# Performance work log

Measured on AMD Instinct MI355X. Metric: run time of the kernel, lower is better.

Reference implementation:

```python
import jax, jax.numpy as jnp
import numpy as np

N = 1024  # step_num
M = 1024  # state_num
C = 64    # in_channels


def _mlp3(x, w1, b1, w2, b2, w3, b3):
    # LinearStack(3, C, C, out): Linear+ReLU, Linear+ReLU, Linear
    h = jax.nn.relu(x @ w1 + b1)
    h = jax.nn.relu(h @ w2 + b2)
    return h @ w3 + b3


def setup_inputs() -> dict:
    key = jax.random.key(0)
    ks = jax.random.split(key, 10)
    s = 1.0 / np.sqrt(C)
    return {
        'step_x': jax.random.normal(ks[0], (N, C), jnp.float32),
        'state_x': jax.random.normal(ks[1], (M, C), jnp.float32),
        'pre_w1': jax.random.normal(ks[2], (C, C), jnp.float32) * s,
        'pre_b1': jnp.zeros((C,), jnp.float32),
        'pre_w2': jax.random.normal(ks[3], (C, C), jnp.float32) * s,
        'pre_b2': jnp.zeros((C,), jnp.float32),
        'pre_w3': jax.random.normal(ks[4], (C, C), jnp.float32) * s,
        'pre_b3': jnp.zeros((C,), jnp.float32),
        'post_w1': jax.random.normal(ks[5], (C, C), jnp.float32) * s,
        'post_b1': jnp.zeros((C,), jnp.float32),
        'post_w2': jax.random.normal(ks[6], (C, C), jnp.float32) * s,
        'post_b2': jnp.zeros((C,), jnp.float32),
        'post_w3': jax.random.normal(ks[7], (C, 2), jnp.float32) * s,
        'post_b3': jnp.zeros((2,), jnp.float32),
    }


def reference(step_x, state_x,
              pre_w1, pre_b1, pre_w2, pre_b2, pre_w3, pre_b3,
              post_w1, post_b1, post_w2, post_b2, post_w3, post_b3):
    # pre-compare MLP on both node sets
    sx = _mlp3(step_x, pre_w1, pre_b1, pre_w2, pre_b2, pre_w3, pre_b3)   # [N,C]
    tx = _mlp3(state_x, pre_w1, pre_b1, pre_w2, pre_b2, pre_w3, pre_b3)  # [M,C]
    n, c = sx.shape
    m = tx.shape[0]

    # step-step pairwise compare ('add') + post-compare -> [N,N,2]
    pair_ss = (sx[:, None, :] + sx[None, :, :]).reshape(n * n, c)
    logits_ss = _mlp3(pair_ss, post_w1, post_b1, post_w2, post_b2,
                      post_w3, post_b3).reshape(n, n, 2)

    # step-state pairwise compare + post-compare -> [N,M,2]
    pair_st = (sx[:, None, :] + tx[None, :, :]).reshape(n * m, c)
    logits_st = _mlp3(pair_st, post_w1, post_b1, post_w2, post_b2,
                      post_w3, post_b3).reshape(n, m, 2)

    # mutual-argmax bipartite matching on sigmoid(match logits)
    match = jax.nn.sigmoid(logits_st[..., 0])                 # [N,M]
    col_arg = jnp.argmax(match, axis=0)                       # [M]
    mask_c = (jnp.arange(n)[:, None] == col_arg[None, :]).astype(match.dtype)
    s1 = match * mask_c
    row_arg = jnp.argmax(s1, axis=1)                          # [N]
    mask_r = (jnp.arange(m)[None, :] == row_arg[:, None]).astype(s1.dtype)
    matched_scores = s1 * mask_r                              # [N,M]

    return logits_ss, logits_st, matched_scores
```

## Files before the change

### kernel.cpp

```cpp
#include <hip/hip_runtime.h>
#include <math.h>

namespace {

constexpr int N_ = 1024;
constexpr int M_ = 1024;
constexpr int C_ = 64;

typedef _Float16 f16x8 __attribute__((ext_vector_type(8)));
typedef __fp16 fp16x2 __attribute__((ext_vector_type(2)));
typedef float f32x4 __attribute__((ext_vector_type(4)));
static_assert(sizeof(f16x8) == 16, "f16x8 must be 4 VGPRs");

__device__ __forceinline__ float sig(float x) { return 1.0f / (1.0f + expf(-x)); }

__device__ __forceinline__ unsigned flipbits(float f) {
    unsigned u = __float_as_uint(f);
    return u ^ (0x80000000u | (unsigned)((int)u >> 31));
}
__device__ __forceinline__ float unflipbits(unsigned k) {
    unsigned u = (k & 0x80000000u) ? (k ^ 0x80000000u) : ~k;
    return __uint_as_float(u);
}
__device__ __forceinline__ unsigned long long packlogit(float v, unsigned idx) {
    return ((unsigned long long)flipbits(v) << 32) | (unsigned)(0xFFFFFFFFu - idx);
}
__device__ __forceinline__ unsigned long long packpos(float v, unsigned idx) {
    return ((unsigned long long)__float_as_uint(v) << 32) | (unsigned)(0xFFFFFFFFu - idx);
}
__device__ __forceinline__ unsigned long long shflx64(unsigned long long v, int m) {
    unsigned lo = __shfl_xor((unsigned)v, m);
    unsigned hi = __shfl_xor((unsigned)(v >> 32), m);
    return ((unsigned long long)hi << 32) | lo;
}

__global__ __launch_bounds__(256) void pre_prep_kernel(
    const float* __restrict__ step_x, const float* __restrict__ state_x,
    const float* __restrict__ w1, const float* __restrict__ b1,
    const float* __restrict__ w2, const float* __restrict__ b2,
    const float* __restrict__ w3, const float* __restrict__ b3,
    const float* __restrict__ pw1, const float* __restrict__ pw2,
    float* __restrict__ U, _Float16* __restrict__ w2T,
    unsigned long long* __restrict__ rowbest)
{
    const int t = threadIdx.x;
    if (blockIdx.x == 128) {
        for (int e = t; e < C_ * C_; e += 256) {
            int k = e >> 6, c = e & 63;
            w2T[c * 64 + k] = (_Float16)pw2[e];
        }
        for (int e = t; e < 1024; e += 256) rowbest[e] = 0ull;
        return;
    }

    __shared__ float XA[16][C_ + 1];
    __shared__ float XB[16][C_ + 1];
    __shared__ float W[C_ * C_];
    __shared__ float Bv[C_];

    const int c = t & 63;
    const int rg = t >> 6;
    const int rbase = blockIdx.x * 16;

    const float* src_g = (rbase < N_) ? (step_x + (size_t)rbase * C_)
                                      : (state_x + (size_t)(rbase - N_) * C_);
    {
        int row = t >> 4, k4 = (t & 15) << 2;
        float4 v = *reinterpret_cast<const float4*>(src_g + row * C_ + k4);
        XA[row][k4 + 0] = v.x; XA[row][k4 + 1] = v.y;
        XA[row][k4 + 2] = v.z; XA[row][k4 + 3] = v.w;
    }

    const float* Ws[4] = {w1, w2, w3, pw1};
    const float* Bs[4] = {b1, b2, b3, nullptr};

    float (*sA)[C_ + 1] = XA;
    float (*sB)[C_ + 1] = XB;

    for (int layer = 0; layer < 4; ++layer) {
        __syncthreads();
        for (int e = t; e < C_ * C_ / 4; e += 256)
            reinterpret_cast<float4*>(W)[e] =
                reinterpret_cast<const float4*>(Ws[layer])[e];
        if (t < C_) Bv[t] = (layer == 3) ? 0.0f : Bs[layer][t];
        __syncthreads();
        const bool relu = (layer < 2);
        #pragma unroll
        for (int q = 0; q < 4; ++q) {
            const int row = rg * 4 + q;
            float acc = Bv[c];
            #pragma unroll 8
            for (int k = 0; k < C_; ++k)
                acc = fmaf(sA[row][k], W[k * C_ + c], acc);
            sB[row][c] = relu ? fmaxf(acc, 0.0f) : acc;
        }
        float (*tmp)[C_ + 1] = sA; sA = sB; sB = tmp;
    }
    #pragma unroll
    for (int q = 0; q < 4; ++q) {
        const int row = rg * 4 + q;
        U[(size_t)(rbase + row) * C_ + c] = sA[row][c];
    }
}

__global__ __launch_bounds__(256) void pair_kernel(
    const float* __restrict__ U,
    const _Float16* __restrict__ w2T,
    const float* __restrict__ pb1, const float* __restrict__ pb2,
    const float* __restrict__ pw3, const float* __restrict__ pb3,
    float* __restrict__ out, unsigned long long* __restrict__ PT2)
{
    __shared__ float SU[32][68];
    __shared__ float SVB[32][68];
    __shared__ float OUTT[32][33][2];
    __shared__ unsigned long long RED[8][32][2];

    const int t = threadIdx.x;
    const int lane = t & 63;
    const int wave = t >> 6;
    const int wi = wave >> 1, wj = wave & 1;
    const int zz = blockIdx.z;
    const int ibase = blockIdx.y * 32;
    const int jbase = blockIdx.x * 32;

    {
        int r = t >> 3, k0 = (t & 7) * 8;
        const float* up = U + (size_t)(ibase + r) * C_ + k0;
        *reinterpret_cast<float4*>(&SU[r][k0])     = *reinterpret_cast<const float4*>(up);
        *reinterpret_cast<float4*>(&SU[r][k0 + 4]) = *reinterpret_cast<const float4*>(up + 4);
        const float* vp = U + (size_t)((zz ? N_ : 0) + jbase + r) * C_ + k0;
        float4 b0 = *reinterpret_cast<const float4*>(vp);
        float4 b1v = *reinterpret_cast<const float4*>(vp + 4);
        float4 c0 = *reinterpret_cast<const float4*>(pb1 + k0);
        float4 c1 = *reinterpret_cast<const float4*>(pb1 + k0 + 4);
        b0.x += c0.x; b0.y += c0.y; b0.z += c0.z; b0.w += c0.w;
        b1v.x += c1.x; b1v.y += c1.y; b1v.z += c1.z; b1v.w += c1.w;
        *reinterpret_cast<float4*>(&SVB[r][k0])     = b0;
        *reinterpret_cast<float4*>(&SVB[r][k0 + 4]) = b1v;
    }

    const int ch_l = lane & 15;
    const int kg = lane >> 4;

    f16x8 whi[4][2];
    #pragma unroll
    for (int mt = 0; mt < 4; ++mt)
        #pragma unroll
        for (int ks = 0; ks < 2; ++ks)
            whi[mt][ks] = *reinterpret_cast<const f16x8*>(
                w2T + (mt * 16 + ch_l) * 64 + ks * 32 + kg * 8);

    float b2v[16], w30[16], w31[16];
    #pragma unroll
    for (int mt = 0; mt < 4; ++mt)
        #pragma unroll
        for (int r = 0; r < 4; ++r) {
            int ch = mt * 16 + kg * 4 + r;
            b2v[mt * 4 + r] = pb2[ch];
            w30[mt * 4 + r] = pw3[ch * 2];
            w31[mt * 4 + r] = pw3[ch * 2 + 1];
        }
    const float ob0 = pb3[0], ob1 = pb3[1];

    __syncthreads();

    float su[2][8];
    #pragma unroll
    for (int ks = 0; ks < 2; ++ks) {
        int k0 = ks * 32 + kg * 8;
        float4 a = *reinterpret_cast<const float4*>(&SU[wi * 16 + ch_l][k0]);
        float4 b = *reinterpret_cast<const float4*>(&SU[wi * 16 + ch_l][k0 + 4]);
        su[ks][0] = a.x; su[ks][1] = a.y; su[ks][2] = a.z; su[ks][3] = a.w;
        su[ks][4] = b.x; su[ks][5] = b.y; su[ks][6] = b.z; su[ks][7] = b.w;
    }

    for (int jj = 0; jj < 16; ++jj) {
        const int jr = wj * 16 + jj;
        f16x8 bhi[2];
        #pragma unroll
        for (int ks = 0; ks < 2; ++ks) {
            int k0 = ks * 32 + kg * 8;
            float4 a = *reinterpret_cast<const float4*>(&SVB[jr][k0]);
            float4 b = *reinterpret_cast<const float4*>(&SVB[jr][k0 + 4]);
            float sv[8] = {a.x, a.y, a.z, a.w, b.x, b.y, b.z, b.w};
            union { f16x8 v; fp16x2 h2[4]; } bu;
            #pragma unroll
            for (int m = 0; m < 4; ++m) {
                float x0 = fmaxf(su[ks][2 * m]     + sv[2 * m],     0.0f);
                float x1 = fmaxf(su[ks][2 * m + 1] + sv[2 * m + 1], 0.0f);
                bu.h2[m] = __builtin_amdgcn_cvt_pkrtz(x0, x1);
            }
            bhi[ks] = bu.v;
        }
        f32x4 ah[4];
        #pragma unroll
        for (int mt = 0; mt < 4; ++mt)
            ah[mt] = f32x4{b2v[4 * mt], b2v[4 * mt + 1], b2v[4 * mt + 2], b2v[4 * mt + 3]};
        #pragma unroll
        for (int ks = 0; ks < 2; ++ks)
            #pragma unroll
            for (int mt = 0; mt < 4; ++mt)
                ah[mt] = __builtin_amdgcn_mfma_f32_16x16x32_f16(whi[mt][ks], bhi[ks], ah[mt], 0, 0, 0);
        float p0 = 0.0f, p1 = 0.0f;
        #pragma unroll
        for (int mt = 0; mt < 4; ++mt)
            #pragma unroll
            for (int r = 0; r < 4; ++r) {
                float g = fmaxf(ah[mt][r], 0.0f);
                p0 = fmaf(g, w30[4 * mt + r], p0);
                p1 = fmaf(g, w31[4 * mt + r], p1);
            }
        p0 += __shfl_xor(p0, 16); p0 += __shfl_xor(p0, 32);
        p1 += __shfl_xor(p1, 16); p1 += __shfl_xor(p1, 32);
        if (lane < 16) {
            OUTT[wi * 16 + lane][wj * 16 + jj][0] = p0 + ob0;
            OUTT[wi * 16 + lane][wj * 16 + jj][1] = p1 + ob1;
        }
    }
    __syncthreads();
    {
        float* obase = out + (size_t)zz * (2ull * N_ * M_);
        int r = t >> 3;
        int q0 = (t & 7) * 4;
        int i = ibase + r;
        #pragma unroll
        for (int q = 0; q < 4; ++q) {
            int j = jbase + q0 + q;
            float2 v = *reinterpret_cast<float2*>(&OUTT[r][q0 + q][0]);
            *reinterpret_cast<float2*>(obase + ((size_t)i * M_ + j) * 2) = v;
        }
    }
    if (zz) {
        const int tc = t & 31, tg = t >> 5;
        unsigned long long k1 = 0, k2 = 0;
        #pragma unroll
        for (int q = 0; q < 4; ++q) {
            int r = tg * 4 + q;
            unsigned long long k = packlogit(OUTT[r][tc][0], (unsigned)(ibase + r));
            if (k > k1) { k2 = k1; k1 = k; } else if (k > k2) k2 = k;
        }
        RED[tg][tc][0] = k1; RED[tg][tc][1] = k2;
        for (int h = 4; h > 0; h >>= 1) {
            __syncthreads();
            if (tg < h) {
                unsigned long long a = RED[tg + h][tc][0], b = RED[tg + h][tc][1];
                if (a > k1) { k2 = k1; k1 = a; } else if (a > k2) k2 = a;
                if (b > k1) { k2 = k1; k1 = b; } else if (b > k2) k2 = b;
                RED[tg][tc][0] = k1; RED[tg][tc][1] = k2;
            }
        }
        if (tg == 0) {
            size_t o = ((size_t)blockIdx.y * M_ + (jbase + tc)) * 2;
            PT2[o] = k1; PT2[o + 1] = k2;
        }
    }
}

__global__ __launch_bounds__(64) void colfinal_kernel(
    const unsigned long long* __restrict__ PT2,
    const float* __restrict__ U, const float* __restrict__ pb1,
    const float* __restrict__ pw2, const float* __restrict__ pb2,
    const float* __restrict__ pw3, const float* __restrict__ pb3,
    unsigned long long* __restrict__ rowbest)
{
    __shared__ float h1s[64];
    const int j = blockIdx.x;
    const int lane = threadIdx.x;

    unsigned long long k1 = PT2[((size_t)(lane >> 1) * M_ + j) * 2 + (lane & 1)];
    unsigned long long k2 = 0;
    #pragma unroll
    for (int m = 1; m < 64; m <<= 1) {
        unsigned long long a = shflx64(k1, m), b = shflx64(k2, m);
        if (a > k1) { k2 = k1; k1 = a; } else if (a > k2) k2 = a;
        if (b > k1) { k2 = k1; k1 = b; } else if (b > k2) k2 = b;
    }
    int ids[2];
    ids[0] = (int)(0xFFFFFFFFu - (unsigned)(k1 & 0xFFFFFFFFull));
    ids[1] = (int)(0xFFFFFFFFu - (unsigned)(k2 & 0xFFFFFFFFull));
    float v1 = unflipbits((unsigned)(k1 >> 32));
    float v2 = unflipbits((unsigned)(k2 >> 32));
    const int nc = (v1 - v2 < 8e-3f) ? 2 : 1;

    float logits[2] = {0.0f, 0.0f};
    for (int cnd = 0; cnd < nc; ++cnd) {
        int i = ids[cnd];
        h1s[lane] = fmaxf(U[(size_t)i * C_ + lane] + U[(size_t)(N_ + j) * C_ + lane] + pb1[lane], 0.0f);
        __syncthreads();
        float acc = pb2[lane];
        #pragma unroll 8
        for (int k = 0; k < 64; ++k)
            acc = fmaf(h1s[k], pw2[k * 64 + lane], acc);
        float p = fmaxf(acc, 0.0f) * pw3[lane * 2];
        #pragma unroll
        for (int m = 1; m < 64; m <<= 1) p += __shfl_xor(p, m);
        logits[cnd] = p + pb3[0];
        __syncthreads();
    }
    int wi; float wp;
    if (nc == 1) { wi = ids[0]; wp = logits[0]; }
    else if (logits[0] > logits[1]) { wi = ids[0]; wp = logits[0]; }
    else if (logits[1] > logits[0]) { wi = ids[1]; wp = logits[1]; }
    else { wi = min(ids[0], ids[1]); wp = logits[0]; }
    if (lane == 0)
        atomicMax(&rowbest[wi], packpos(sig(wp), (unsigned)j));
}

__global__ __launch_bounds__(256) void zscatter_kernel(
    const unsigned long long* __restrict__ rowbest, float* __restrict__ matched)
{
    int i = blockIdx.x;
    int t = threadIdx.x;
    *reinterpret_cast<float4*>(matched + (size_t)i * M_ + t * 4) =
        float4{0.0f, 0.0f, 0.0f, 0.0f};
    __syncthreads();
    if (t == 0) {
        unsigned long long key = rowbest[i];
        if (key) {
            unsigned j = 0xFFFFFFFFu - (unsigned)(key & 0xFFFFFFFFull);
            matched[(size_t)i * M_ + j] = __uint_as_float((unsigned)(key >> 32));
        }
    }
}

}

extern "C" void kernel_launch(void* const* d_in, const int* in_sizes, int n_in,
                              void* d_out, int out_size, void* d_ws, size_t ws_size,
                              hipStream_t stream)
{
    const float* step_x  = (const float*)d_in[0];
    const float* state_x = (const float*)d_in[1];
    const float* pre_w1  = (const float*)d_in[2];
    const float* pre_b1  = (const float*)d_in[3];
    const float* pre_w2  = (const float*)d_in[4];
    const float* pre_b2  = (const float*)d_in[5];
    const float* pre_w3  = (const float*)d_in[6];
    const float* pre_b3  = (const float*)d_in[7];
    const float* post_w1 = (const float*)d_in[8];
    const float* post_b1 = (const float*)d_in[9];
    const float* post_w2 = (const float*)d_in[10];
    const float* post_b2 = (const float*)d_in[11];
    const float* post_w3 = (const float*)d_in[12];
    const float* post_b3 = (const float*)d_in[13];

    float* out     = (float*)d_out;
    float* matched = out + 4ull * N_ * M_;

    float* U = (float*)d_ws;
    unsigned long long* rowbest = (unsigned long long*)((char*)d_ws + 2048ull * 64 * 4);

    char* ms = (char*)matched;
    unsigned long long* PT2 = (unsigned long long*)ms;
    _Float16*  w2T     = (_Float16*)(ms + 512 * 1024);

    hipLaunchKernelGGL(pre_prep_kernel, dim3(129), dim3(256), 0, stream,
        step_x, state_x, pre_w1, pre_b1, pre_w2, pre_b2, pre_w3, pre_b3,
        post_w1, post_w2, U, w2T, rowbest);
    hipLaunchKernelGGL(pair_kernel, dim3(32, 32, 2), dim3(256), 0, stream,
        U, w2T, post_b1, post_b2, post_w3, post_b3, out, PT2);
    hipLaunchKernelGGL(colfinal_kernel, dim3(1024), dim3(64), 0, stream,
        PT2, U, post_b1, post_w2, post_b2, post_w3, post_b3, rowbest);
    hipLaunchKernelGGL(zscatter_kernel, dim3(1024), dim3(256), 0, stream,
        rowbest, matched);
}
```

Baseline: 147.2 us.

## Fuse all four stages into one persistent kernel with grid barriers

Merges the pre-MLP, pairwise MFMA, column-final and scatter kernels into a single 512-block persistent kernel separated by atomic grid-wide barriers, with a memset to clear barrier counters and rowbest. Each block now handles both the step-step and step-state tiles for a shared U row tile, reusing the loaded SU data, and colfinal packs four columns per block. The aim is to remove launch gaps and tail effects between the small kernels. In exchange it relies on all 512 blocks being co-resident for the spin barriers, and it lowers parallelism in the pre-MLP and pair stages. The colfinal step also now always evaluates two candidates instead of branching on the gap.

Measured after the change: 427.1 us. 2.9x slower.

```diff
diff --git a/kernel.cpp b/kernel.cpp
--- a/kernel.cpp
+++ b/kernel.cpp
@@ -6,11 +6,11 @@
 constexpr int N_ = 1024;
 constexpr int M_ = 1024;
 constexpr int C_ = 64;
+constexpr unsigned NBLK = 512;
 
 typedef _Float16 f16x8 __attribute__((ext_vector_type(8)));
 typedef __fp16 fp16x2 __attribute__((ext_vector_type(2)));
 typedef float f32x4 __attribute__((ext_vector_type(4)));
-static_assert(sizeof(f16x8) == 16, "f16x8 must be 4 VGPRs");
 
 __device__ __forceinline__ float sig(float x) { return 1.0f / (1.0f + expf(-x)); }
 
@@ -34,291 +34,298 @@
     return ((unsigned long long)hi << 32) | lo;
 }
 
-__global__ __launch_bounds__(256) void pre_prep_kernel(
+__device__ __forceinline__ void gridbar(unsigned* bar, unsigned target) {
+    __syncthreads();
+    if (threadIdx.x == 0) {
+        __threadfence();
+        __hip_atomic_fetch_add(bar, 1u, __ATOMIC_RELEASE, __HIP_MEMORY_SCOPE_AGENT);
+        while (__hip_atomic_load(bar, __ATOMIC_ACQUIRE, __HIP_MEMORY_SCOPE_AGENT) < target)
+            __builtin_amdgcn_s_sleep(4);
+        __threadfence();
+    }
+    __syncthreads();
+}
+
+struct SmemA { float XA[4][C_ + 1]; float XB[4][C_ + 1]; float W[C_ * C_]; float Bv[C_]; };
+struct SmemB {
+    float SU[32][68];
+    float SVB[2][32][68];
+    float OUTT[32][33][2];
+    unsigned long long RED[8][32][2];
+};
+struct SmemC { float h1s[4][C_]; };
+union Smem { SmemA a; SmemB b; SmemC c; };
+
+__global__ __launch_bounds__(256, 4) void fused_kernel(
     const float* __restrict__ step_x, const float* __restrict__ state_x,
     const float* __restrict__ w1, const float* __restrict__ b1,
     const float* __restrict__ w2, const float* __restrict__ b2,
     const float* __restrict__ w3, const float* __restrict__ b3,
-    const float* __restrict__ pw1, const float* __restrict__ pw2,
+    const float* __restrict__ pw1, const float* __restrict__ pb1,
+    const float* __restrict__ pw2, const float* __restrict__ pb2,
+    const float* __restrict__ pw3, const float* __restrict__ pb3,
     float* __restrict__ U, _Float16* __restrict__ w2T,
-    unsigned long long* __restrict__ rowbest)
+    unsigned long long* __restrict__ rowbest,
+    float* __restrict__ out, unsigned long long* __restrict__ PT2,
+    unsigned* __restrict__ bar)
 {
+    __shared__ Smem sm;
     const int t = threadIdx.x;
-    if (blockIdx.x == 128) {
-        for (int e = t; e < C_ * C_; e += 256) {
-            int k = e >> 6, c = e & 63;
-            w2T[c * 64 + k] = (_Float16)pw2[e];
-        }
-        for (int e = t; e < 1024; e += 256) rowbest[e] = 0ull;
-        return;
-    }
-
-    __shared__ float XA[16][C_ + 1];
-    __shared__ float XB[16][C_ + 1];
-    __shared__ float W[C_ * C_];
-    __shared__ float Bv[C_];
-
-    const int c = t & 63;
-    const int rg = t >> 6;
-    const int rbase = blockIdx.x * 16;
-
-    const float* src_g = (rbase < N_) ? (step_x + (size_t)rbase * C_)
-                                      : (state_x + (size_t)(rbase - N_) * C_);
+    const int bid = blockIdx.x;
+
     {
-        int row = t >> 4, k4 = (t & 15) << 2;
-        float4 v = *reinterpret_cast<const float4*>(src_g + row * C_ + k4);
-        XA[row][k4 + 0] = v.x; XA[row][k4 + 1] = v.y;
-        XA[row][k4 + 2] = v.z; XA[row][k4 + 3] = v.w;
-    }
-
-    const float* Ws[4] = {w1, w2, w3, pw1};
-    const float* Bs[4] = {b1, b2, b3, nullptr};
-
-    float (*sA)[C_ + 1] = XA;
-    float (*sB)[C_ + 1] = XB;
-
-    for (int layer = 0; layer < 4; ++layer) {
-        __syncthreads();
-        for (int e = t; e < C_ * C_ / 4; e += 256)
-            reinterpret_cast<float4*>(W)[e] =
-                reinterpret_cast<const float4*>(Ws[layer])[e];
-        if (t < C_) Bv[t] = (layer == 3) ? 0.0f : Bs[layer][t];
-        __syncthreads();
-        const bool relu = (layer < 2);
-        #pragma unroll
-        for (int q = 0; q < 4; ++q) {
-            const int row = rg * 4 + q;
-            float acc = Bv[c];
+        SmemA& A = sm.a;
+        const int r0 = bid * 4;
+        if (t < 64) {
+            int rr = t >> 4, k4 = (t & 15) << 2;
+            int row = r0 + rr;
+            const float* src = (row < N_) ? (step_x + (size_t)row * C_ + k4)
+                                          : (state_x + (size_t)(row - N_) * C_ + k4);
+            float4 v = *reinterpret_cast<const float4*>(src);
+            A.XA[rr][k4 + 0] = v.x; A.XA[rr][k4 + 1] = v.y;
+            A.XA[rr][k4 + 2] = v.z; A.XA[rr][k4 + 3] = v.w;
+        }
+        if (bid >= 480 && bid < 496) {
+            int e = (bid - 480) * 256 + t;
+            w2T[(e & 63) * 64 + (e >> 6)] = (_Float16)pw2[e];
+        }
+
+        const float* Ws[4] = {w1, w2, w3, pw1};
+        const float* Bs[4] = {b1, b2, b3, nullptr};
+        float (*sA)[C_ + 1] = A.XA;
+        float (*sB)[C_ + 1] = A.XB;
+        const int c = t & 63;
+        const int row = t >> 6;
+        for (int layer = 0; layer < 4; ++layer) {
+            __syncthreads();
+            for (int e = t; e < C_ * C_ / 4; e += 256)
+                reinterpret_cast<float4*>(A.W)[e] =
+                    reinterpret_cast<const float4*>(Ws[layer])[e];
+            if (t < C_) A.Bv[t] = (layer == 3) ? 0.0f : Bs[layer][t];
+            __syncthreads();
+            float acc = A.Bv[c];
             #pragma unroll 8
             for (int k = 0; k < C_; ++k)
-                acc = fmaf(sA[row][k], W[k * C_ + c], acc);
-            sB[row][c] = relu ? fmaxf(acc, 0.0f) : acc;
-        }
-        float (*tmp)[C_ + 1] = sA; sA = sB; sB = tmp;
-    }
-    #pragma unroll
-    for (int q = 0; q < 4; ++q) {
-        const int row = rg * 4 + q;
-        U[(size_t)(rbase + row) * C_ + c] = sA[row][c];
-    }
-}
-
-__global__ __launch_bounds__(256) void pair_kernel(
-    const float* __restrict__ U,
-    const _Float16* __restrict__ w2T,
-    const float* __restrict__ pb1, const float* __restrict__ pb2,
-    const float* __restrict__ pw3, const float* __restrict__ pb3,
-    float* __restrict__ out, unsigned long long* __restrict__ PT2)
-{
-    __shared__ float SU[32][68];
-    __shared__ float SVB[32][68];
-    __shared__ float OUTT[32][33][2];
-    __shared__ unsigned long long RED[8][32][2];
-
-    const int t = threadIdx.x;
-    const int lane = t & 63;
-    const int wave = t >> 6;
-    const int wi = wave >> 1, wj = wave & 1;
-    const int zz = blockIdx.z;
-    const int ibase = blockIdx.y * 32;
-    const int jbase = blockIdx.x * 32;
+                acc = fmaf(sA[row][k], A.W[k * C_ + c], acc);
+            sB[row][c] = (layer < 2) ? fmaxf(acc, 0.0f) : acc;
+            float (*tmp)[C_ + 1] = sA; sA = sB; sB = tmp;
+        }
+        U[(size_t)(r0 + row) * C_ + c] = sA[row][c];
+    }
+    gridbar(bar + 0, NBLK);
 
     {
-        int r = t >> 3, k0 = (t & 7) * 8;
-        const float* up = U + (size_t)(ibase + r) * C_ + k0;
-        *reinterpret_cast<float4*>(&SU[r][k0])     = *reinterpret_cast<const float4*>(up);
-        *reinterpret_cast<float4*>(&SU[r][k0 + 4]) = *reinterpret_cast<const float4*>(up + 4);
-        const float* vp = U + (size_t)((zz ? N_ : 0) + jbase + r) * C_ + k0;
-        float4 b0 = *reinterpret_cast<const float4*>(vp);
-        float4 b1v = *reinterpret_cast<const float4*>(vp + 4);
-        float4 c0 = *reinterpret_cast<const float4*>(pb1 + k0);
-        float4 c1 = *reinterpret_cast<const float4*>(pb1 + k0 + 4);
-        b0.x += c0.x; b0.y += c0.y; b0.z += c0.z; b0.w += c0.w;
-        b1v.x += c1.x; b1v.y += c1.y; b1v.z += c1.z; b1v.w += c1.w;
-        *reinterpret_cast<float4*>(&SVB[r][k0])     = b0;
-        *reinterpret_cast<float4*>(&SVB[r][k0 + 4]) = b1v;
-    }
-
-    const int ch_l = lane & 15;
-    const int kg = lane >> 4;
-
-    f16x8 whi[4][2];
-    #pragma unroll
-    for (int mt = 0; mt < 4; ++mt)
-        #pragma unroll
-        for (int ks = 0; ks < 2; ++ks)
-            whi[mt][ks] = *reinterpret_cast<const f16x8*>(
-                w2T + (mt * 16 + ch_l) * 64 + ks * 32 + kg * 8);
-
-    float b2v[16], w30[16], w31[16];
-    #pragma unroll
-    for (int mt = 0; mt < 4; ++mt)
-        #pragma unroll
-        for (int r = 0; r < 4; ++r) {
-            int ch = mt * 16 + kg * 4 + r;
-            b2v[mt * 4 + r] = pb2[ch];
-            w30[mt * 4 + r] = pw3[ch * 2];
-            w31[mt * 4 + r] = pw3[ch * 2 + 1];
-        }
-    const float ob0 = pb3[0], ob1 = pb3[1];
-
-    __syncthreads();
-
-    float su[2][8];
-    #pragma unroll
-    for (int ks = 0; ks < 2; ++ks) {
-        int k0 = ks * 32 + kg * 8;
-        float4 a = *reinterpret_cast<const float4*>(&SU[wi * 16 + ch_l][k0]);
-        float4 b = *reinterpret_cast<const float4*>(&SU[wi * 16 + ch_l][k0 + 4]);
-        su[ks][0] = a.x; su[ks][1] = a.y; su[ks][2] = a.z; su[ks][3] = a.w;
-        su[ks][4] = b.x; su[ks][5] = b.y; su[ks][6] = b.z; su[ks][7] = b.w;
-    }
-
-    for (int jj = 0; jj < 16; ++jj) {
-        const int jr = wj * 16 + jj;
-        f16x8 bhi[2];
-        #pragma unroll
-        for (int ks = 0; ks < 2; ++ks) {
-            int k0 = ks * 32 + kg * 8;
-            float4 a = *reinterpret_cast<const float4*>(&SVB[jr][k0]);
-            float4 b = *reinterpret_cast<const float4*>(&SVB[jr][k0 + 4]);
-            float sv[8] = {a.x, a.y, a.z, a.w, b.x, b.y, b.z, b.w};
-            union { f16x8 v; fp16x2 h2[4]; } bu;
+        SmemB& B = sm.b;
+        const int lane = t & 63;
+        const int wave = t >> 6;
+        const int wi = wave >> 1, wj = wave & 1;
+        const int ch_l = lane & 15;
+        const int kg = lane >> 4;
+
+        f16x8 whi[4][2];
+        #pragma unroll
+        for (int mt = 0; mt < 4; ++mt)
             #pragma unroll
-            for (int m = 0; m < 4; ++m) {
-                float x0 = fmaxf(su[ks][2 * m]     + sv[2 * m],     0.0f);
-                float x1 = fmaxf(su[ks][2 * m + 1] + sv[2 * m + 1], 0.0f);
-                bu.h2[m] = __builtin_amdgcn_cvt_pkrtz(x0, x1);
-            }
-            bhi[ks] = bu.v;
-        }
-        f32x4 ah[4];
-        #pragma unroll
-        for (int mt = 0; mt < 4; ++mt)
-            ah[mt] = f32x4{b2v[4 * mt], b2v[4 * mt + 1], b2v[4 * mt + 2], b2v[4 * mt + 3]};
-        #pragma unroll
-        for (int ks = 0; ks < 2; ++ks)
-            #pragma unroll
-            for (int mt = 0; mt < 4; ++mt)
-                ah[mt] = __builtin_amdgcn_mfma_f32_16x16x32_f16(whi[mt][ks], bhi[ks], ah[mt], 0, 0, 0);
-        float p0 = 0.0f, p1 = 0.0f;
+            for (int ks = 0; ks < 2; ++ks)
+                whi[mt][ks] = *reinterpret_cast<const f16x8*>(
+                    w2T + (mt * 16 + ch_l) * 64 + ks * 32 + kg * 8);
+
+        float b2v[16], w30[16], w31[16];
         #pragma unroll
         for (int mt = 0; mt < 4; ++mt)
             #pragma unroll
             for (int r = 0; r < 4; ++r) {
-                float g = fmaxf(ah[mt][r], 0.0f);
-                p0 = fmaf(g, w30[4 * mt + r], p0);
-                p1 = fmaf(g, w31[4 * mt + r], p1);
-            }
-        p0 += __shfl_xor(p0, 16); p0 += __shfl_xor(p0, 32);
-        p1 += __shfl_xor(p1, 16); p1 += __shfl_xor(p1, 32);
-        if (lane < 16) {
-            OUTT[wi * 16 + lane][wj * 16 + jj][0] = p0 + ob0;
-            OUTT[wi * 16 + lane][wj * 16 + jj][1] = p1 + ob1;
-        }
-    }
-    __syncthreads();
+                int ch = mt * 16 + kg * 4 + r;
+                b2v[mt * 4 + r] = pb2[ch];
+                w30[mt * 4 + r] = pw3[ch * 2];
+                w31[mt * 4 + r] = pw3[ch * 2 + 1];
+            }
+        const float ob0 = pb3[0], ob1 = pb3[1];
+
+        for (int p = 0; p < 2; ++p) {
+            const int tp = bid + p * 512;
+            const int ibase = (tp >> 5) * 32;
+            const int jbase = (tp & 31) * 32;
+
+            __syncthreads();
+            {
+                const int r = t >> 3, k0 = (t & 7) * 8;
+                const float* up = U + (size_t)(ibase + r) * C_ + k0;
+                *reinterpret_cast<float4*>(&B.SU[r][k0])     = *reinterpret_cast<const float4*>(up);
+                *reinterpret_cast<float4*>(&B.SU[r][k0 + 4]) = *reinterpret_cast<const float4*>(up + 4);
+                float4 c0 = *reinterpret_cast<const float4*>(pb1 + k0);
+                float4 c1 = *reinterpret_cast<const float4*>(pb1 + k0 + 4);
+                #pragma unroll
+                for (int zzv = 0; zzv < 2; ++zzv) {
+                    const float* vp = U + (size_t)(zzv * N_ + jbase + r) * C_ + k0;
+                    float4 b0 = *reinterpret_cast<const float4*>(vp);
+                    float4 b1v = *reinterpret_cast<const float4*>(vp + 4);
+                    b0.x += c0.x; b0.y += c0.y; b0.z += c0.z; b0.w += c0.w;
+                    b1v.x += c1.x; b1v.y += c1.y; b1v.z += c1.z; b1v.w += c1.w;
+                    *reinterpret_cast<float4*>(&B.SVB[zzv][r][k0])     = b0;
+                    *reinterpret_cast<float4*>(&B.SVB[zzv][r][k0 + 4]) = b1v;
+                }
+            }
+            __syncthreads();
+
+            float su[2][8];
+            #pragma unroll
+            for (int ks = 0; ks < 2; ++ks) {
+                int k0 = ks * 32 + kg * 8;
+                float4 a = *reinterpret_cast<const float4*>(&B.SU[wi * 16 + ch_l][k0]);
+                float4 b = *reinterpret_cast<const float4*>(&B.SU[wi * 16 + ch_l][k0 + 4]);
+                su[ks][0] = a.x; su[ks][1] = a.y; su[ks][2] = a.z; su[ks][3] = a.w;
+                su[ks][4] = b.x; su[ks][5] = b.y; su[ks][6] = b.z; su[ks][7] = b.w;
+            }
+
+            for (int zzv = 0; zzv < 2; ++zzv) {
+                if (zzv) __syncthreads();
+                for (int jj = 0; jj < 16; ++jj) {
+                    const int jr = wj * 16 + jj;
+                    f16x8 bhi[2];
+                    #pragma unroll
+                    for (int ks = 0; ks < 2; ++ks) {
+                        int k0 = ks * 32 + kg * 8;
+                        float4 a = *reinterpret_cast<const float4*>(&B.SVB[zzv][jr][k0]);
+                        float4 b = *reinterpret_cast<const float4*>(&B.SVB[zzv][jr][k0 + 4]);
+                        float sv[8] = {a.x, a.y, a.z, a.w, b.x, b.y, b.z, b.w};
+                        union { f16x8 v; fp16x2 h2[4]; } bu;
+                        #pragma unroll
+                        for (int m = 0; m < 4; ++m) {
+                            float x0 = fmaxf(su[ks][2 * m]     + sv[2 * m],     0.0f);
+                            float x1 = fmaxf(su[ks][2 * m + 1] + sv[2 * m + 1], 0.0f);
+                            bu.h2[m] = __builtin_amdgcn_cvt_pkrtz(x0, x1);
+                        }
+                        bhi[ks] = bu.v;
+                    }
+                    f32x4 ah[4];
+                    #pragma unroll
+                    for (int mt = 0; mt < 4; ++mt)
+                        ah[mt] = f32x4{b2v[4 * mt], b2v[4 * mt + 1], b2v[4 * mt + 2], b2v[4 * mt + 3]};
+                    #pragma unroll
+                    for (int ks = 0; ks < 2; ++ks)
+                        #pragma unroll
+                        for (int mt = 0; mt < 4; ++mt)
+                            ah[mt] = __builtin_amdgcn_mfma_f32_16x16x32_f16(whi[mt][ks], bhi[ks], ah[mt], 0, 0, 0);
+                    float p0 = 0.0f, p1 = 0.0f;
+                    #pragma unroll
+                    for (int mt = 0; mt < 4; ++mt)
+                        #pragma unroll
+                        for (int r = 0; r < 4; ++r) {
+                            float g = fmaxf(ah[mt][r], 0.0f);
+                            p0 = fmaf(g, w30[4 * mt + r], p0);
+                            p1 = fmaf(g, w31[4 * mt + r], p1);
+                        }
+                    p0 += __shfl_xor(p0, 16); p0 += __shfl_xor(p0, 32);
+                    p1 += __shfl_xor(p1, 16); p1 += __shfl_xor(p1, 32);
+                    if (lane < 16) {
+                        B.OUTT[wi * 16 + lane][wj * 16 + jj][0] = p0 + ob0;
+                        B.OUTT[wi * 16 + lane][wj * 16 + jj][1] = p1 + ob1;
+                    }
+                }
+                __syncthreads();
+                {
+                    float* obase = out + (size_t)zzv * (2ull * N_ * M_);
+                    int r = t >> 3;
+                    int q0 = (t & 7) * 4;
+                    int i = ibase + r;
+                    #pragma unroll
+                    for (int q = 0; q < 4; ++q) {
+                        int j = jbase + q0 + q;
+                        float2 v = *reinterpret_cast<float2*>(&B.OUTT[r][q0 + q][0]);
+                        *reinterpret_cast<float2*>(obase + ((size_t)i * M_ + j) * 2) = v;
+                    }
+                }
+                if (zzv) {
+                    const int tc = t & 31, tg = t >> 5;
+                    unsigned long long k1 = 0, k2 = 0;
+                    #pragma unroll
+                    for (int q = 0; q < 4; ++q) {
+                        int r = tg * 4 + q;
+                        unsigned long long k = packlogit(B.OUTT[r][tc][0], (unsigned)(ibase + r));
+                        if (k > k1) { k2 = k1; k1 = k; } else if (k > k2) k2 = k;
+                    }
+                    B.RED[tg][tc][0] = k1; B.RED[tg][tc][1] = k2;
+                    for (int h = 4; h > 0; h >>= 1) {
+                        __syncthreads();
+                        if (tg < h) {
+                            unsigned long long a = B.RED[tg + h][tc][0], b = B.RED[tg + h][tc][1];
+                            if (a > k1) { k2 = k1; k1 = a; } else if (a > k2) k2 = a;
+                            if (b > k1) { k2 = k1; k1 = b; } else if (b > k2) k2 = b;
+                            B.RED[tg][tc][0] = k1; B.RED[tg][tc][1] = k2;
+                        }
+                    }
+                    if (tg == 0) {
+                        size_t o = ((size_t)(tp >> 5) * M_ + (jbase + tc)) * 2;
+                        PT2[o] = k1; PT2[o + 1] = k2;
+                    }
+                }
+            }
+        }
+    }
+    gridbar(bar + 1, NBLK);
+
+    if (bid < 256) {
+        SmemC& Cc = sm.c;
+        const int w = t >> 6, lane = t & 63;
+        const int j = bid * 4 + w;
+
+        unsigned long long k1 = PT2[((size_t)(lane >> 1) * M_ + j) * 2 + (lane & 1)];
+        unsigned long long k2 = 0;
+        #pragma unroll
+        for (int m = 1; m < 64; m <<= 1) {
+            unsigned long long a = shflx64(k1, m), b = shflx64(k2, m);
+            if (a > k1) { k2 = k1; k1 = a; } else if (a > k2) k2 = a;
+            if (b > k1) { k2 = k1; k1 = b; } else if (b > k2) k2 = b;
+        }
+        int ids[2];
+        ids[0] = (int)(0xFFFFFFFFu - (unsigned)(k1 & 0xFFFFFFFFull));
+        int i2 = (int)(0xFFFFFFFFu - (unsigned)(k2 & 0xFFFFFFFFull));
+        float v1 = unflipbits((unsigned)(k1 >> 32));
+        float v2 = unflipbits((unsigned)(k2 >> 32));
+        ids[1] = (v1 - v2 < 8e-3f) ? i2 : ids[0];
+
+        float logits[2];
+        #pragma unroll
+        for (int cnd = 0; cnd < 2; ++cnd) {
+            int i = ids[cnd];
+            Cc.h1s[w][lane] = fmaxf(U[(size_t)i * C_ + lane] + U[(size_t)(N_ + j) * C_ + lane] + pb1[lane], 0.0f);
+            __syncthreads();
+            float acc = pb2[lane];
+            #pragma unroll 8
+            for (int k = 0; k < 64; ++k)
+                acc = fmaf(Cc.h1s[w][k], pw2[k * 64 + lane], acc);
+            float p = fmaxf(acc, 0.0f) * pw3[lane * 2];
+            #pragma unroll
+            for (int m = 1; m < 64; m <<= 1) p += __shfl_xor(p, m);
+            logits[cnd] = p + pb3[0];
+            __syncthreads();
+        }
+        int wi2; float wp;
+        if (logits[0] > logits[1])      { wi2 = ids[0]; wp = logits[0]; }
+        else if (logits[1] > logits[0]) { wi2 = ids[1]; wp = logits[1]; }
+        else                            { wi2 = min(ids[0], ids[1]); wp = logits[0]; }
+        if (lane == 0)
+            atomicMax(&rowbest[wi2], packpos(sig(wp), (unsigned)j));
+    }
+    gridbar(bar + 2, NBLK);
+
     {
-        float* obase = out + (size_t)zz * (2ull * N_ * M_);
-        int r = t >> 3;
-        int q0 = (t & 7) * 4;
-        int i = ibase + r;
-        #pragma unroll
-        for (int q = 0; q < 4; ++q) {
-            int j = jbase + q0 + q;
-            float2 v = *reinterpret_cast<float2*>(&OUTT[r][q0 + q][0]);
-            *reinterpret_cast<float2*>(obase + ((size_t)i * M_ + j) * 2) = v;
-        }
-    }
-    if (zz) {
-        const int tc = t & 31, tg = t >> 5;
-        unsigned long long k1 = 0, k2 = 0;
-        #pragma unroll
-        for (int q = 0; q < 4; ++q) {
-            int r = tg * 4 + q;
-            unsigned long long k = packlogit(OUTT[r][tc][0], (unsigned)(ibase + r));
-            if (k > k1) { k2 = k1; k1 = k; } else if (k > k2) k2 = k;
-        }
-        RED[tg][tc][0] = k1; RED[tg][tc][1] = k2;
-        for (int h = 4; h > 0; h >>= 1) {
-            __syncthreads();
-            if (tg < h) {
-                unsigned long long a = RED[tg + h][tc][0], b = RED[tg + h][tc][1];
-                if (a > k1) { k2 = k1; k1 = a; } else if (a > k2) k2 = a;
-                if (b > k1) { k2 = k1; k1 = b; } else if (b > k2) k2 = b;
-                RED[tg][tc][0] = k1; RED[tg][tc][1] = k2;
-            }
-        }
-        if (tg == 0) {
-            size_t o = ((size_t)blockIdx.y * M_ + (jbase + tc)) * 2;
-            PT2[o] = k1; PT2[o + 1] = k2;
-        }
-    }
-}
-
-__global__ __launch_bounds__(64) void colfinal_kernel(
-    const unsigned long long* __restrict__ PT2,
-    const float* __restrict__ U, const float* __restrict__ pb1,
-    const float* __restrict__ pw2, const float* __restrict__ pb2,
-    const float* __restrict__ pw3, const float* __restrict__ pb3,
-    unsigned long long* __restrict__ rowbest)
-{
-    __shared__ float h1s[64];
-    const int j = blockIdx.x;
-    const int lane = threadIdx.x;
-
-    unsigned long long k1 = PT2[((size_t)(lane >> 1) * M_ + j) * 2 + (lane & 1)];
-    unsigned long long k2 = 0;
-    #pragma unroll
-    for (int m = 1; m < 64; m <<= 1) {
-        unsigned long long a = shflx64(k1, m), b = shflx64(k2, m);
-        if (a > k1) { k2 = k1; k1 = a; } else if (a > k2) k2 = a;
-        if (b > k1) { k2 = k1; k1 = b; } else if (b > k2) k2 = b;
-    }
-    int ids[2];
-    ids[0] = (int)(0xFFFFFFFFu - (unsigned)(k1 & 0xFFFFFFFFull));
-    ids[1] = (int)(0xFFFFFFFFu - (unsigned)(k2 & 0xFFFFFFFFull));
-    float v1 = unflipbits((unsigned)(k1 >> 32));
-    float v2 = unflipbits((unsigned)(k2 >> 32));
-    const int nc = (v1 - v2 < 8e-3f) ? 2 : 1;
-
-    float logits[2] = {0.0f, 0.0f};
-    for (int cnd = 0; cnd < nc; ++cnd) {
-        int i = ids[cnd];
-        h1s[lane] = fmaxf(U[(size_t)i * C_ + lane] + U[(size_t)(N_ + j) * C_ + lane] + pb1[lane], 0.0f);
+        float* matched = out + 4ull * N_ * M_;
+        #pragma unroll
+        for (int rr = 0; rr < 2; ++rr) {
+            int i = bid * 2 + rr;
+            *reinterpret_cast<float4*>(matched + (size_t)i * M_ + t * 4) =
+                float4{0.0f, 0.0f, 0.0f, 0.0f};
+        }
         __syncthreads();
-        float acc = pb2[lane];
-        #pragma unroll 8
-        for (int k = 0; k < 64; ++k)
-            acc = fmaf(h1s[k], pw2[k * 64 + lane], acc);
-        float p = fmaxf(acc, 0.0f) * pw3[lane * 2];
-        #pragma unroll
-        for (int m = 1; m < 64; m <<= 1) p += __shfl_xor(p, m);
-        logits[cnd] = p + pb3[0];
-        __syncthreads();
-    }
-    int wi; float wp;
-    if (nc == 1) { wi = ids[0]; wp = logits[0]; }
-    else if (logits[0] > logits[1]) { wi = ids[0]; wp = logits[0]; }
-    else if (logits[1] > logits[0]) { wi = ids[1]; wp = logits[1]; }
-    else { wi = min(ids[0], ids[1]); wp = logits[0]; }
-    if (lane == 0)
-        atomicMax(&rowbest[wi], packpos(sig(wp), (unsigned)j));
-}
-
-__global__ __launch_bounds__(256) void zscatter_kernel(
-    const unsigned long long* __restrict__ rowbest, float* __restrict__ matched)
-{
-    int i = blockIdx.x;
-    int t = threadIdx.x;
-    *reinterpret_cast<float4*>(matched + (size_t)i * M_ + t * 4) =
-        float4{0.0f, 0.0f, 0.0f, 0.0f};
-    __syncthreads();
-    if (t == 0) {
-        unsigned long long key = rowbest[i];
-        if (key) {
-            unsigned j = 0xFFFFFFFFu - (unsigned)(key & 0xFFFFFFFFull);
-            matched[(size_t)i * M_ + j] = __uint_as_float((unsigned)(key >> 32));
+        if (t < 2) {
+            int i = bid * 2 + t;
+            unsigned long long key = rowbest[i];
+            if (key) {
+                unsigned j = 0xFFFFFFFFu - (unsigned)(key & 0xFFFFFFFFull);
+                matched[(size_t)i * M_ + j] = __uint_as_float((unsigned)(key >> 32));
+            }
         }
     }
 }
@@ -348,19 +355,16 @@
     float* matched = out + 4ull * N_ * M_;
 
     float* U = (float*)d_ws;
-    unsigned long long* rowbest = (unsigned long long*)((char*)d_ws + 2048ull * 64 * 4);
-
-    char* ms = (char*)matched;
-    unsigned long long* PT2 = (unsigned long long*)ms;
-    _Float16*  w2T     = (_Float16*)(ms + 512 * 1024);
-
-    hipLaunchKernelGGL(pre_prep_kernel, dim3(129), dim3(256), 0, stream,
+    unsigned long long* rowbest = (unsigned long long*)((char*)d_ws + 512 * 1024);
+    unsigned* bar = (unsigned*)((char*)d_ws + 520 * 1024);
+
+    unsigned long long* PT2 = (unsigned long long*)matched;
+    _Float16* w2T = (_Float16*)((char*)matched + 512 * 1024);
+
+    hipMemsetAsync((char*)d_ws + 512 * 1024, 0, 8 * 1024 + 16, stream);
+
+    hipLaunchKernelGGL(fused_kernel, dim3(NBLK), dim3(256), 0, stream,
         step_x, state_x, pre_w1, pre_b1, pre_w2, pre_b2, pre_w3, pre_b3,
-        post_w1, post_w2, U, w2T, rowbest);
-    hipLaunchKernelGGL(pair_kernel, dim3(32, 32, 2), dim3(256), 0, stream,
-        U, w2T, post_b1, post_b2, post_w3, post_b3, out, PT2);
-    hipLaunchKernelGGL(colfinal_kernel, dim3(1024), dim3(64), 0, stream,
-        PT2, U, post_b1, post_w2, post_b2, post_w3, post_b3, rowbest);
-    hipLaunchKernelGGL(zscatter_kernel, dim3(1024), dim3(256), 0, stream,
-        rowbest, matched);
-}
+        post_w1, post_b1, post_w2, post_b2, post_w3, post_b3,
+        U, w2T, rowbest, out, PT2, bar);
+}
```
